# Optimization experiments

Hardware: AMD Instinct MI355X
Metric: run time of the kernel (lower is better)

Reference implementation:

```python
import jax, jax.numpy as jnp
import numpy as np

N_NODES = 524288
N_EDGES = 2097152
N_GRAPHS = 16384
COMP_DIM = 3539
PROT_DIM = 384
GNN_HID = 64
G_EMB = 128
HID = 256


def setup_inputs() -> dict:
    key = jax.random.key(0)
    ks = jax.random.split(key, 16)
    def lin(k, fan_in, fan_out):
        b = 1.0 / np.sqrt(fan_in)
        kw, kb = jax.random.split(k)
        return (jax.random.uniform(kw, (fan_in, fan_out), jnp.float32, -b, b),
                jax.random.uniform(kb, (fan_out,), jnp.float32, -b, b))
    W1, b1 = lin(ks[0], 1, GNN_HID)
    W2, b2 = lin(ks[1], GNN_HID, GNN_HID)
    Wg, bg = lin(ks[2], GNN_HID, G_EMB)
    Wf1, bf1 = lin(ks[3], G_EMB + COMP_DIM + PROT_DIM, HID)
    Wf2, bf2 = lin(ks[4], HID, 1)
    node_x = jax.random.normal(ks[5], (N_NODES, 1), jnp.float32)
    compound_feat = jax.random.normal(ks[6], (N_GRAPHS, COMP_DIM), jnp.float32)
    protein_feat = jax.random.normal(ks[7], (N_GRAPHS, PROT_DIM), jnp.float32)
    edge_index = jax.random.randint(ks[8], (2, N_EDGES), 0, N_NODES, jnp.int64 if jax.config.jax_enable_x64 else jnp.int32)
    batch = jnp.sort(jax.random.randint(ks[9], (N_NODES,), 0, N_GRAPHS, jnp.int32))
    return {"node_x": node_x, "compound_feat": compound_feat, "protein_feat": protein_feat,
            "edge_index": edge_index, "batch": batch,
            "W1": W1, "b1": b1, "W2": W2, "b2": b2, "Wg": Wg, "bg": bg,
            "Wf1": Wf1, "bf1": bf1, "Wf2": Wf2, "bf2": bf2}


def _gcn_norm(edge_index, num_nodes):
    # add self-loops, then symmetric normalization (PyG GCNConv default)
    loop = jnp.arange(num_nodes, dtype=edge_index.dtype)
    row = jnp.concatenate([edge_index[0], loop])
    col = jnp.concatenate([edge_index[1], loop])
    deg = jax.ops.segment_sum(jnp.ones_like(col, jnp.float32), col, num_segments=num_nodes)
    dinv = jnp.where(deg > 0, jax.lax.rsqrt(deg), 0.0)
    norm = dinv[row] * dinv[col]
    return row, col, norm


def _gcn_conv(x, W, b, row, col, norm, num_nodes):
    h = x @ W  # [N, out]
    out = jax.ops.segment_sum(norm[:, None] * h[row], col, num_segments=num_nodes)
    return out + b


def reference(node_x, compound_feat, protein_feat, edge_index, batch,
              W1, b1, W2, b2, Wg, bg, Wf1, bf1, Wf2, bf2):
    N = node_x.shape[0]
    B = compound_feat.shape[0]
    row, col, norm = _gcn_norm(edge_index, N)
    x = jax.nn.relu(_gcn_conv(node_x, W1, b1, row, col, norm, N))
    x = jax.nn.relu(_gcn_conv(x, W2, b2, row, col, norm, N))
    # global mean pool per graph
    sums = jax.ops.segment_sum(x, batch, num_segments=B)
    cnts = jax.ops.segment_sum(jnp.ones((N,), jnp.float32), batch, num_segments=B)
    pooled = sums / jnp.maximum(cnts, 1.0)[:, None]
    g = pooled @ Wg + bg  # [B, G_EMB]
    combined = jnp.concatenate([g, compound_feat, protein_feat], axis=1)
    h = jax.nn.relu(combined @ Wf1 + bf1)
    return jax.nn.sigmoid(h @ Wf2 + bf2)
```

## Files before the change

### kernel.cpp

```cpp
#include <hip/hip_runtime.h>

#define NN 524288
#define NE 2097152
#define NG 16384
#define CDIM 3539
#define PDIM 384
#define GH 64
#define GE 128
#define HIDD 256
#define KD (GE + CDIM + PDIM)
#define KP 4096

typedef short bf16x8 __attribute__((ext_vector_type(8)));
typedef unsigned short u16x8 __attribute__((ext_vector_type(8)));
typedef float f32x4 __attribute__((ext_vector_type(4)));

__device__ inline unsigned short f2bf(float f) {
    unsigned int u = __float_as_uint(f);
    u += 0x7FFF + ((u >> 16) & 1);
    return (unsigned short)(u >> 16);
}

__global__ void k_init(int* __restrict__ idg, float* __restrict__ sums) {
    int i = blockIdx.x * blockDim.x + threadIdx.x;
    if (i < NN) idg[i] = 0;
    if (i < NG * GH) sums[i] = 0.0f;
}

__global__ void k_deg(const int* __restrict__ ei, int* __restrict__ idg,
                      int* __restrict__ eseq) {
    int e = blockIdx.x * blockDim.x + threadIdx.x;
    eseq[e] = atomicAdd(&idg[ei[NE + e]], 1);
}

__global__ void k_prep(const float* __restrict__ node_x, const int* __restrict__ idg,
                       float2* __restrict__ f2a, int* __restrict__ ecnt) {
    int n = blockIdx.x * blockDim.x + threadIdx.x;
    int c = idg[n];
    float di = rsqrtf((float)(c + 1));
    f2a[n] = make_float2(di * node_x[n], di);
    ecnt[n] = c;
}

__global__ void k_cnt(const int* __restrict__ batch, float* __restrict__ cnt) {
    int g = blockIdx.x * 256 + threadIdx.x;
    int lo = 0, hi = NN;
    while (lo < hi) { int mid = (lo + hi) >> 1; if (batch[mid] < g) lo = mid + 1; else hi = mid; }
    int lo2 = lo, hi2 = NN;
    while (lo2 < hi2) { int mid = (lo2 + hi2) >> 1; if (batch[mid] < g + 1) lo2 = mid + 1; else hi2 = mid; }
    cnt[g] = (float)(lo2 - lo);
}

__global__ void k_scan1(const int* __restrict__ ecnt, int* __restrict__ bsum) {
    __shared__ int ls[256];
    int t = threadIdx.x;
    ls[t] = ecnt[blockIdx.x * 256 + t];
    __syncthreads();
    for (int d = 128; d > 0; d >>= 1) { if (t < d) ls[t] += ls[t + d]; __syncthreads(); }
    if (t == 0) bsum[blockIdx.x] = ls[0];
}

__global__ void k_scan2(int* __restrict__ bsum) {
    __shared__ int ls[256];
    int t = threadIdx.x;
    int loc[8]; int s = 0;
#pragma unroll
    for (int i = 0; i < 8; i++) { loc[i] = bsum[t * 8 + i]; s += loc[i]; }
    ls[t] = s; __syncthreads();
    for (int d = 1; d < 256; d <<= 1) {
        int add = (t >= d) ? ls[t - d] : 0; __syncthreads();
        ls[t] += add; __syncthreads();
    }
    int run = ls[t] - s;
#pragma unroll
    for (int i = 0; i < 8; i++) { int tmp = loc[i]; bsum[t * 8 + i] = run; run += tmp; }
}

__global__ void k_scan3(const int* __restrict__ ecnt, const int* __restrict__ bsum,
                        int* __restrict__ offs) {
    __shared__ int ls[256];
    int t = threadIdx.x, n = blockIdx.x * 256 + t;
    int v = ecnt[n];
    ls[t] = v; __syncthreads();
    for (int d = 1; d < 256; d <<= 1) {
        int add = (t >= d) ? ls[t - d] : 0; __syncthreads();
        ls[t] += add; __syncthreads();
    }
    offs[n] = bsum[blockIdx.x] + ls[t] - v;
    if (n == 0) offs[NN] = NE;
}

__global__ void k_fill(const int* __restrict__ ei, const int* __restrict__ offs,
                       const int* __restrict__ eseq, int* __restrict__ csr) {
    int e = blockIdx.x * 256 + threadIdx.x;
    int r = ei[e], c = ei[NE + e];
    csr[offs[c] + eseq[e]] = r;
}

__global__ void k_sg(const int* __restrict__ offs, const int* __restrict__ csr,
                     const float2* __restrict__ f2a, float2* __restrict__ sd) {
    int n = blockIdx.x * 256 + threadIdx.x;
    int a = offs[n], b = offs[n + 1];
    float2 me = f2a[n];
    float sum = me.x;
    for (int e = a; e < b; e += 4) {
#pragma unroll
        for (int i = 0; i < 4; i++) {
            int ee = e + i;
            int r = csr[min(ee, b - 1)];
            float v = f2a[r].x;
            sum += (ee < b) ? v : 0.0f;
        }
    }
    sd[n] = make_float2(me.y * sum, me.y);
}

__global__ __launch_bounds__(256) void k_gx2(
        const int* __restrict__ offs, const int* __restrict__ csr,
        const float2* __restrict__ sd, const float* __restrict__ W1,
        const float* __restrict__ b1, const unsigned short* __restrict__ W2T,
        const float* __restrict__ b2, const int* __restrict__ batch,
        float* __restrict__ sums) {
    __shared__ unsigned short aggs[64][72];
    __shared__ float x2s[64][73];
    __shared__ int bloc[64];
    int t = threadIdx.x;
    int wv = t >> 6, lane = t & 63;
    int n0 = blockIdx.x * 64;
    int nw = n0 + wv * 16;
    if (t < 64) bloc[t] = batch[n0 + t];
    float w1j = W1[lane], b1j = b1[lane];
    int nl = nw + (lane & 15);
    int aL = offs[nl], bndL = offs[nl + 1];
    float2 sdL = sd[nl];

    int base   = __shfl(aL, 0, 64);
    int endAll = __shfl(bndL, 15, 64);

#define LOADB(dst, bs) do { int en = (bs) + lane;                        \
    dst = make_float2(0.0f, 0.0f);                                       \
    if (en < endAll) dst = sd[csr[en]]; } while (0)

    int bstart = base;
    float2 vcur, vnxt;
    LOADB(vcur, bstart);
    LOADB(vnxt, bstart + 64);

    for (int i = 0; i < 16; i++) {
        int a    = __shfl(aL, i, 64);
        int bnd  = __shfl(bndL, i, 64);
        float sx = __shfl(sdL.x, i, 64);
        float sy = __shfl(sdL.y, i, 64);
        float acc = sy * fmaxf(fmaf(sx, w1j, b1j), 0.0f);
        for (int e = a; e < bnd; ++e) {
            int slot = e - bstart;
            if (slot >= 64) {
                bstart += 64;
                slot -= 64;
                vcur = vnxt;
                LOADB(vnxt, bstart + 64);
            }
            float vx = __shfl(vcur.x, slot, 64);
            float vy = __shfl(vcur.y, slot, 64);
            acc = fmaf(vy, fmaxf(fmaf(vx, w1j, b1j), 0.0f), acc);
        }
        aggs[wv * 16 + i][lane] = f2bf(sy * acc);
    }
#undef LOADB

    __syncthreads();
    int lg = lane >> 4, lr = lane & 15;
    bf16x8 a0 = *reinterpret_cast<const bf16x8*>(&aggs[wv * 16 + lr][lg * 8]);
    bf16x8 a1 = *reinterpret_cast<const bf16x8*>(&aggs[wv * 16 + lr][32 + lg * 8]);
    f32x4 acc4[4];
#pragma unroll
    for (int jt = 0; jt < 4; jt++) acc4[jt] = (f32x4){0.f, 0.f, 0.f, 0.f};
#pragma unroll
    for (int jt = 0; jt < 4; jt++) {
        bf16x8 b0 = *reinterpret_cast<const bf16x8*>(W2T + (jt * 16 + lr) * GH + lg * 8);
        bf16x8 b1v = *reinterpret_cast<const bf16x8*>(W2T + (jt * 16 + lr) * GH + 32 + lg * 8);
        acc4[jt] = __builtin_amdgcn_mfma_f32_16x16x32_bf16(a0, b0, acc4[jt], 0, 0, 0);
        acc4[jt] = __builtin_amdgcn_mfma_f32_16x16x32_bf16(a1, b1v, acc4[jt], 0, 0, 0);
    }
#pragma unroll
    for (int jt = 0; jt < 4; jt++) {
        float bj = b2[jt * 16 + lr];
#pragma unroll
        for (int r = 0; r < 4; r++)
            x2s[wv * 16 + lg * 4 + r][jt * 16 + lr] = fmaxf(acc4[jt][r] + bj, 0.0f);
    }
    __syncthreads();
    for (int i = wv; i < 64; i += 4) {
        bool isStart = (i == 0) || (bloc[i] != bloc[i - 1]);
        if (isStart) {
            int g = bloc[i];
            float s = 0.0f;
            int k = i;
            do { s += x2s[k][lane]; k++; } while (k < 64 && bloc[k] == g);
            atomicAdd(&sums[g * GH + lane], s);
        }
    }
}

__global__ void k_graph(const float* __restrict__ sums, const float* __restrict__ cnt,
                        const float* __restrict__ Wg, const float* __restrict__ bg,
                        float* __restrict__ gemb) {
    __shared__ float wgs[GH * GE];
    __shared__ float ps[4 * GH];
    int t = threadIdx.x;
    for (int i = t; i < GH * GE; i += 256) wgs[i] = Wg[i];
    int gid = blockIdx.x * 256 + t;
    int g = gid >> 6, j = t & 63, w = t >> 6;
    float c = fmaxf(cnt[g], 1.0f);
    ps[t] = sums[g * GH + j] / c;
    __syncthreads();
    float o0 = bg[j], o1 = bg[GH + j];
#pragma unroll
    for (int k = 0; k < GH; k++) {
        float p = ps[w * GH + k];
        o0 = fmaf(p, wgs[k * GE + j], o0);
        o1 = fmaf(p, wgs[k * GE + GH + j], o1);
    }
    gemb[g * GE + j] = o0;
    gemb[g * GE + GH + j] = o1;
}

__global__ void k_wt(const float* __restrict__ Wf1, unsigned short* __restrict__ WT,
                     const float* __restrict__ W2, unsigned short* __restrict__ W2T) {
    if (blockIdx.x == 1024) {
        int t = threadIdx.x;
        for (int i = 0; i < 16; i++) {
            int idx = t * 16 + i;
            int j = idx >> 6, k = idx & 63;
            W2T[j * GH + k] = f2bf(W2[k * GH + j]);
        }
        return;
    }
    __shared__ float tl[32][33];
    int bk = blockIdx.x & 127;
    int bn = blockIdx.x >> 7;
    int tx = threadIdx.x & 31, ty = threadIdx.x >> 5;
    int k0 = bk * 32, n0 = bn * 32;
#pragma unroll
    for (int i = 0; i < 4; i++) {
        int k = k0 + ty + i * 8;
        tl[ty + i * 8][tx] = (k < KD) ? Wf1[k * HIDD + n0 + tx] : 0.0f;
    }
    __syncthreads();
#pragma unroll
    for (int i = 0; i < 4; i++) {
        int n = n0 + ty + i * 8;
        WT[n * KP + k0 + tx] = f2bf(tl[tx][ty + i * 8]);
    }
}

__global__ void k_comb(const float* __restrict__ gemb, const float* __restrict__ comp,
                       const float* __restrict__ prot, unsigned short* __restrict__ comb) {
    size_t t = ((size_t)blockIdx.x * 256 + threadIdx.x) * 8;
    int g = (int)(t >> 12), k0 = (int)(t & (KP - 1));
    u16x8 r;
#pragma unroll
    for (int i = 0; i < 8; i++) {
        int k = k0 + i;
        float v = 0.0f;
        if (k < GE) v = gemb[g * GE + k];
        else if (k < GE + CDIM) v = comp[(size_t)g * CDIM + (k - GE)];
        else if (k < KD) v = prot[g * PDIM + (k - GE - CDIM)];
        r[i] = f2bf(v);
    }
    *reinterpret_cast<u16x8*>(comb + t) = r;
}

typedef const __attribute__((address_space(1))) void gas_void;
typedef __attribute__((address_space(3))) void las_void;

__global__ __launch_bounds__(256) void k_gemm_mfma(
        const unsigned short* __restrict__ WT, const unsigned short* __restrict__ comb,
        const float* __restrict__ bf1, const float* __restrict__ Wf2,
        const float* __restrict__ bf2, float* __restrict__ out) {
    __shared__ unsigned short ldsA[2][256 * 32];
    __shared__ unsigned short ldsB[2][32 * 32];
    __shared__ float red[32];
    int t = threadIdx.x;
    int wv = t >> 6, lane = t & 63;
    int lg = lane >> 4, lr = lane & 15;
    int g0 = blockIdx.x * 32;
    int nbase = wv * 64;

    int rowp = lane >> 2;
    int kp = (lane & 3) * 8;

    if (t < 32) red[t] = 0.0f;

    f32x4 acc[4][2];
#pragma unroll
    for (int i = 0; i < 4; i++)
#pragma unroll
        for (int j = 0; j < 2; j++) acc[i][j] = (f32x4){0.f, 0.f, 0.f, 0.f};

#define STAGE(buf, k0) do {                                                                  \
    _Pragma("unroll")                                                                        \
    for (int i = 0; i < 4; i++)                                                              \
        __builtin_amdgcn_global_load_lds(                                                    \
            (gas_void*)(WT + (size_t)(wv * 64 + i * 16 + rowp) * KP + (k0) + kp),            \
            (las_void*)(&ldsA[buf][(wv * 64 + i * 16) * 32]), 16, 0, 0);                     \
    if (wv < 2)                                                                              \
        __builtin_amdgcn_global_load_lds(                                                    \
            (gas_void*)(comb + (size_t)(g0 + wv * 16 + rowp) * KP + (k0) + kp),              \
            (las_void*)(&ldsB[buf][(wv * 16) * 32]), 16, 0, 0);                              \
} while (0)

    STAGE(0, 0);
    __syncthreads();
#pragma unroll 1
    for (int s = 0; s < 128; ++s) {
        int cur = s & 1;
        if (s < 127) STAGE(cur ^ 1, (s + 1) * 32);
        bf16x8 a[4], b[2];
#pragma unroll
        for (int nt = 0; nt < 4; nt++)
            a[nt] = *reinterpret_cast<const bf16x8*>(&ldsA[cur][(nbase + nt * 16 + lr) * 32 + lg * 8]);
#pragma unroll
        for (int gt = 0; gt < 2; gt++)
            b[gt] = *reinterpret_cast<const bf16x8*>(&ldsB[cur][(gt * 16 + lr) * 32 + lg * 8]);
#pragma unroll
        for (int nt = 0; nt < 4; nt++)
#pragma unroll
            for (int gt = 0; gt < 2; gt++)
                acc[nt][gt] = __builtin_amdgcn_mfma_f32_16x16x32_bf16(a[nt], b[gt], acc[nt][gt], 0, 0, 0);
        __syncthreads();
    }
#undef STAGE

    float bf2c = bf2[0];
#pragma unroll
    for (int gt = 0; gt < 2; gt++) {
        float pv = 0.0f;
#pragma unroll
        for (int nt = 0; nt < 4; nt++) {
            int nb = nbase + nt * 16 + lg * 4;
#pragma unroll
            for (int r = 0; r < 4; r++) {
                float h = fmaxf(acc[nt][gt][r] + bf1[nb + r], 0.0f);
                pv = fmaf(h, Wf2[nb + r], pv);
            }
        }
        pv += __shfl_xor(pv, 16);
        pv += __shfl_xor(pv, 32);
        if (lane < 16) atomicAdd(&red[gt * 16 + lane], pv);
    }
    __syncthreads();
    if (t < 32) out[g0 + t] = 1.0f / (1.0f + expf(-(red[t] + bf2c)));
}

extern "C" void kernel_launch(void* const* d_in, const int* in_sizes, int n_in,
                              void* d_out, int out_size, void* d_ws, size_t ws_size,
                              hipStream_t stream) {
    const float* node_x = (const float*)d_in[0];
    const float* comp   = (const float*)d_in[1];
    const float* prot   = (const float*)d_in[2];
    const int*   ei     = (const int*)d_in[3];
    const int*   batch  = (const int*)d_in[4];
    const float* W1  = (const float*)d_in[5];
    const float* b1  = (const float*)d_in[6];
    const float* W2  = (const float*)d_in[7];
    const float* b2  = (const float*)d_in[8];
    const float* Wg  = (const float*)d_in[9];
    const float* bg  = (const float*)d_in[10];
    const float* Wf1 = (const float*)d_in[11];
    const float* bf1 = (const float*)d_in[12];
    const float* Wf2 = (const float*)d_in[13];
    const float* bf2 = (const float*)d_in[14];
    float* out = (float*)d_out;

    char* W = (char*)d_ws;
    unsigned short* comb = (unsigned short*)W;
    int*    idg     = (int*)(W + 0);
    float2* f2a     = (float2*)(W + 2097152);
    float2* sd      = (float2*)(W + 6291456);
    int*    ecnt    = (int*)(W + 10485760);
    int*    offs    = (int*)(W + 12582912);
    int*    bsum    = (int*)(W + 16777728);
    int*    csr     = (int*)(W + 16786432);
    float*  sums    = (float*)(W + 25175040);
    float*  cnt     = (float*)(W + 29369344);
    int*    eseq    = (int*)(W + 33554432);
    float*  gemb    = (float*)(W + 134217728);
    unsigned short* WT  = (unsigned short*)(W + 142606336);
    unsigned short* W2T = (unsigned short*)(W + 144703488);

    k_init<<<4096, 256, 0, stream>>>(idg, sums);
    k_wt<<<1025, 256, 0, stream>>>(Wf1, WT, W2, W2T);
    k_deg<<<NE / 256, 256, 0, stream>>>(ei, idg, eseq);
    k_prep<<<NN / 256, 256, 0, stream>>>(node_x, idg, f2a, ecnt);
    k_cnt<<<NG / 256, 256, 0, stream>>>(batch, cnt);
    k_scan1<<<NN / 256, 256, 0, stream>>>(ecnt, bsum);
    k_scan2<<<1, 256, 0, stream>>>(bsum);
    k_scan3<<<NN / 256, 256, 0, stream>>>(ecnt, bsum, offs);
    k_fill<<<NE / 256, 256, 0, stream>>>(ei, offs, eseq, csr);
    k_sg<<<NN / 256, 256, 0, stream>>>(offs, csr, f2a, sd);
    k_gx2<<<NN / 64, 256, 0, stream>>>(offs, csr, sd, W1, b1, W2T, b2, batch, sums);
    k_graph<<<NG * GH / 256, 256, 0, stream>>>(sums, cnt, Wg, bg, gemb);
    k_comb<<<NG * KP / (256 * 8), 256, 0, stream>>>(gemb, comp, prot, comb);
    k_gemm_mfma<<<NG / 32, 256, 0, stream>>>(WT, comb, bf1, Wf2, bf2, out);
}
```

Baseline: 563.9 us.

## Fuse feature concat and bf16 conversion into the MFMA GEMM B-tile staging

Removes the separate k_comb kernel, which concatenated graph embedding, compound and protein features into a padded bf16 buffer. The GEMM now reads the fp32 sources directly, converts them to bf16 in registers and writes them to a padded LDS tile, with a register prefetch two stages ahead. This avoids writing and re-reading a large intermediate buffer. In exchange, the B loads use unaligned 16-byte reads (the compound rows have an odd stride), and the GEMM main loop carries extra per-thread ALU and branching. The K loop is also trimmed to the stages that cover the real K dimension.

```diff
diff --git a/kernel.cpp b/kernel.cpp
--- a/kernel.cpp
+++ b/kernel.cpp
@@ -12,7 +12,6 @@
 #define KP 4096
 
 typedef short bf16x8 __attribute__((ext_vector_type(8)));
-typedef unsigned short u16x8 __attribute__((ext_vector_type(8)));
 typedef float f32x4 __attribute__((ext_vector_type(4)));
 
 __device__ inline unsigned short f2bf(float f) {
@@ -254,32 +253,18 @@
     }
 }
 
-__global__ void k_comb(const float* __restrict__ gemb, const float* __restrict__ comp,
-                       const float* __restrict__ prot, unsigned short* __restrict__ comb) {
-    size_t t = ((size_t)blockIdx.x * 256 + threadIdx.x) * 8;
-    int g = (int)(t >> 12), k0 = (int)(t & (KP - 1));
-    u16x8 r;
-#pragma unroll
-    for (int i = 0; i < 8; i++) {
-        int k = k0 + i;
-        float v = 0.0f;
-        if (k < GE) v = gemb[g * GE + k];
-        else if (k < GE + CDIM) v = comp[(size_t)g * CDIM + (k - GE)];
-        else if (k < KD) v = prot[g * PDIM + (k - GE - CDIM)];
-        r[i] = f2bf(v);
-    }
-    *reinterpret_cast<u16x8*>(comb + t) = r;
-}
-
 typedef const __attribute__((address_space(1))) void gas_void;
 typedef __attribute__((address_space(3))) void las_void;
 
+#define BSTRIDE 40
+
 __global__ __launch_bounds__(256) void k_gemm_mfma(
-        const unsigned short* __restrict__ WT, const unsigned short* __restrict__ comb,
+        const unsigned short* __restrict__ WT, const float* __restrict__ gemb,
+        const float* __restrict__ comp, const float* __restrict__ prot,
         const float* __restrict__ bf1, const float* __restrict__ Wf2,
         const float* __restrict__ bf2, float* __restrict__ out) {
     __shared__ unsigned short ldsA[2][256 * 32];
-    __shared__ unsigned short ldsB[2][32 * 32];
+    __shared__ unsigned short ldsB[2][32 * BSTRIDE];
     __shared__ float red[32];
     int t = threadIdx.x;
     int wv = t >> 6, lane = t & 63;
@@ -290,6 +275,12 @@
     int rowp = lane >> 2;
     int kp = (lane & 3) * 8;
 
+    int brow = t >> 3;
+    int bkk = (t & 7) * 4;
+    const float* gsrc = gemb + (size_t)(g0 + brow) * GE;
+    const float* csrc = comp + (size_t)(g0 + brow) * CDIM - GE;
+    const float* psrc = prot + (size_t)(g0 + brow) * PDIM - (GE + CDIM);
+
     if (t < 32) red[t] = 0.0f;
 
     f32x4 acc[4][2];
@@ -298,31 +289,60 @@
 #pragma unroll
         for (int j = 0; j < 2; j++) acc[i][j] = (f32x4){0.f, 0.f, 0.f, 0.f};
 
-#define STAGE(buf, k0) do {                                                                  \
+#define STAGEA(buf, k0) do {                                                                 \
     _Pragma("unroll")                                                                        \
     for (int i = 0; i < 4; i++)                                                              \
         __builtin_amdgcn_global_load_lds(                                                    \
             (gas_void*)(WT + (size_t)(wv * 64 + i * 16 + rowp) * KP + (k0) + kp),            \
             (las_void*)(&ldsA[buf][(wv * 64 + i * 16) * 32]), 16, 0, 0);                     \
-    if (wv < 2)                                                                              \
-        __builtin_amdgcn_global_load_lds(                                                    \
-            (gas_void*)(comb + (size_t)(g0 + wv * 16 + rowp) * KP + (k0) + kp),              \
-            (las_void*)(&ldsB[buf][(wv * 16) * 32]), 16, 0, 0);                              \
 } while (0)
 
-    STAGE(0, 0);
+#define LOADB4(dst, S) do { int gk = (S) * 32 + bkk;                                         \
+    if ((S) <= 3)        __builtin_memcpy(&dst, gsrc + gk, 16);                              \
+    else if ((S) <= 113) __builtin_memcpy(&dst, csrc + gk, 16);                              \
+    else if ((S) >= 115 && (S) <= 125) __builtin_memcpy(&dst, psrc + gk, 16);                \
+    else if ((S) >= 127) { dst[0] = dst[1] = dst[2] = dst[3] = 0.0f; }                       \
+    else {                                                                                   \
+        _Pragma("unroll")                                                                    \
+        for (int q = 0; q < 4; q++) {                                                        \
+            int k = gk + q; float x = 0.0f;                                                  \
+            if (k < GE) x = gsrc[k];                                                         \
+            else if (k < GE + CDIM) x = csrc[k];                                             \
+            else if (k < KD) x = psrc[k];                                                    \
+            dst[q] = x;                                                                      \
+        }                                                                                    \
+    }                                                                                        \
+} while (0)
+
+#define WRITEB(buf, v) do {                                                                  \
+    unsigned long long pk = (unsigned long long)f2bf(v[0])                                   \
+        | ((unsigned long long)f2bf(v[1]) << 16)                                             \
+        | ((unsigned long long)f2bf(v[2]) << 32)                                             \
+        | ((unsigned long long)f2bf(v[3]) << 48);                                            \
+    *reinterpret_cast<unsigned long long*>(&ldsB[buf][brow * BSTRIDE + bkk]) = pk;           \
+} while (0)
+
+    f32x4 vb, vbn;
+    LOADB4(vb, 0);
+    STAGEA(0, 0);
+    WRITEB(0, vb);
+    LOADB4(vbn, 1);
     __syncthreads();
 #pragma unroll 1
-    for (int s = 0; s < 128; ++s) {
+    for (int s = 0; s < 127; ++s) {
         int cur = s & 1;
-        if (s < 127) STAGE(cur ^ 1, (s + 1) * 32);
+        if (s < 126) {
+            STAGEA(cur ^ 1, (s + 1) * 32);
+            WRITEB(cur ^ 1, vbn);
+            if (s < 125) LOADB4(vbn, s + 2);
+        }
         bf16x8 a[4], b[2];
 #pragma unroll
         for (int nt = 0; nt < 4; nt++)
             a[nt] = *reinterpret_cast<const bf16x8*>(&ldsA[cur][(nbase + nt * 16 + lr) * 32 + lg * 8]);
 #pragma unroll
         for (int gt = 0; gt < 2; gt++)
-            b[gt] = *reinterpret_cast<const bf16x8*>(&ldsB[cur][(gt * 16 + lr) * 32 + lg * 8]);
+            b[gt] = *reinterpret_cast<const bf16x8*>(&ldsB[cur][(gt * 16 + lr) * BSTRIDE + lg * 8]);
 #pragma unroll
         for (int nt = 0; nt < 4; nt++)
 #pragma unroll
@@ -330,7 +350,9 @@
                 acc[nt][gt] = __builtin_amdgcn_mfma_f32_16x16x32_bf16(a[nt], b[gt], acc[nt][gt], 0, 0, 0);
         __syncthreads();
     }
-#undef STAGE
+#undef STAGEA
+#undef LOADB4
+#undef WRITEB
 
     float bf2c = bf2[0];
 #pragma unroll
@@ -374,7 +396,6 @@
     float* out = (float*)d_out;
 
     char* W = (char*)d_ws;
-    unsigned short* comb = (unsigned short*)W;
     int*    idg     = (int*)(W + 0);
     float2* f2a     = (float2*)(W + 2097152);
     float2* sd      = (float2*)(W + 6291456);
@@ -401,6 +422,5 @@
     k_sg<<<NN / 256, 256, 0, stream>>>(offs, csr, f2a, sd);
     k_gx2<<<NN / 64, 256, 0, stream>>>(offs, csr, sd, W1, b1, W2T, b2, batch, sums);
     k_graph<<<NG * GH / 256, 256, 0, stream>>>(sums, cnt, Wg, bg, gemb);
-    k_comb<<<NG * KP / (256 * 8), 256, 0, stream>>>(gemb, comp, prot, comb);
-    k_gemm_mfma<<<NG / 32, 256, 0, stream>>>(WT, comb, bf1, Wf2, bf2, out);
-}
+    k_gemm_mfma<<<NG / 32, 256, 0, stream>>>(WT, gemb, comp, prot, bf1, Wf2, bf2, out);
+}
```

Result: faster. 491.7 us (-12.8%).
